# Performance work log

Hardware: AMD Instinct MI355X
Metric: run time of the kernel (lower is better)

The kernel has to match this reference:

```python
import jax, jax.numpy as jnp
import numpy as np

WEIGHT_DIM = 1024
NUM_HEADS = 16
B, L, H = 2, 2048, 1024


def setup_inputs() -> dict:
    key = jax.random.key(0)
    k1, k2, k3, k4, k5 = jax.random.split(key, 5)
    scale = 1.0 / np.sqrt(H)
    return {
        "input": jax.random.normal(k1, (B, L, H), dtype=jnp.float32),
        "attention_mask": jnp.ones((B, L), dtype=jnp.float32),
        "wq": jax.random.normal(k2, (H, WEIGHT_DIM), dtype=jnp.float32) * scale,
        "wk": jax.random.normal(k3, (H, WEIGHT_DIM), dtype=jnp.float32) * scale,
        "wv": jax.random.normal(k4, (H, WEIGHT_DIM), dtype=jnp.float32) * scale,
        "wo": jax.random.normal(k5, (WEIGHT_DIM, H), dtype=jnp.float32) * scale,
    }


def _split_heads(x):
    # (B, L, D) -> (B, nh, L, D/nh)
    b, l, d = x.shape
    return x.reshape(b, l, NUM_HEADS, d // NUM_HEADS).transpose(0, 2, 1, 3)


def reference(input, attention_mask, wq, wk, wv, wo):
    b, l, h = input.shape
    q = _split_heads(input @ wq)
    k = _split_heads(input @ wk)
    v = _split_heads(input @ wv)

    # logits: (B, nh, L, L)
    logit = jnp.einsum("bhqd,bhkd->bhqk", q, k)

    # future mask: strictly upper triangular = 1 (masked)
    f_mask = jnp.triu(jnp.ones((l, l), dtype=jnp.float32), k=1)
    # pad mask: 1 where either position is pad
    p = attention_mask[:, :, None] * attention_mask[:, None, :]  # (B, L, L)
    p_mask = 1.0 - p
    # combined mask (logical_or of booleans expressed as float max)
    mask = jnp.maximum(f_mask[None, None, :, :], p_mask[:, None, :, :])

    # faithful to source: add dtype.min * mask BEFORE dividing by sqrt(d)
    logit = logit + jnp.finfo(logit.dtype).min * mask
    attn = jax.nn.softmax(logit / jnp.sqrt(jnp.float32(WEIGHT_DIM)), axis=-1)

    ctx = jnp.einsum("bhqk,bhkd->bhqd", attn, v)
    ctx = ctx.transpose(0, 2, 1, 3).reshape(b, l, WEIGHT_DIM)
    return ctx @ wo
```

## Files before the change

### kernel.cpp

```cpp
#include <hip/hip_runtime.h>


#define L_SEQ  2048
#define NBATCH 2
#define HDIM   1024
#define NHEADS 16
#define DHEAD  64
#define MB     (L_SEQ)
#define PADK   72
#define PADP   72

using frag_ab = __attribute__((ext_vector_type(8))) short;
using frag_cd = __attribute__((ext_vector_type(4))) float;

__device__ inline unsigned short f2bf(float f) {
  unsigned u = __float_as_uint(f);
  u += 0x7fffu + ((u >> 16) & 1u);
  return (unsigned short)(u >> 16);
}
__device__ inline float bf2f(unsigned short h) {
  return __uint_as_float(((unsigned)h) << 16);
}
__device__ inline float fexp2(float x) {
#if __has_builtin(__builtin_amdgcn_exp2f)
  return __builtin_amdgcn_exp2f(x);
#else
  return exp2f(x);
#endif
}

typedef __attribute__((address_space(1))) unsigned int glb_u32;
typedef __attribute__((address_space(3))) unsigned int lds_u32;
__device__ inline void gload16(const void* g, void* l) {
  __builtin_amdgcn_global_load_lds((glb_u32*)g, (lds_u32*)l, 16, 0, 0);
}

__global__ __launch_bounds__(256) void convx(
    const float* __restrict__ X, unsigned short* __restrict__ Y) {
  size_t idx = ((size_t)blockIdx.x * 256 + threadIdx.x) * 8;
  float4 a = *(const float4*)(X + idx);
  float4 b = *(const float4*)(X + idx + 4);
  union { uint4 v; unsigned short u[8]; } o;
  o.u[0] = f2bf(a.x); o.u[1] = f2bf(a.y); o.u[2] = f2bf(a.z); o.u[3] = f2bf(a.w);
  o.u[4] = f2bf(b.x); o.u[5] = f2bf(b.y); o.u[6] = f2bf(b.z); o.u[7] = f2bf(b.w);
  *(uint4*)(Y + idx) = o.v;
}

__global__ __launch_bounds__(256) void transw(
    const float* wq, const float* wk, const float* wv, const float* wo,
    unsigned short* WT) {
  __shared__ unsigned short t[32][33];
  const float* s = (blockIdx.z == 0) ? wq : (blockIdx.z == 1) ? wk
                 : (blockIdx.z == 2) ? wv : wo;
  unsigned short* d = WT + (size_t)blockIdx.z * HDIM * HDIM;
  int k0 = blockIdx.y * 32, n0 = blockIdx.x * 32;
  int tx = threadIdx.x, ty = threadIdx.y;
  for (int i = ty; i < 32; i += 8)
    t[i][tx] = f2bf(s[(size_t)(k0 + i) * HDIM + n0 + tx]);
  __syncthreads();
  for (int i = ty; i < 32; i += 8)
    d[(size_t)(n0 + i) * HDIM + k0 + tx] = t[tx][i];
}

template<int C_BF16, int VT_OUT>
__global__ __launch_bounds__(256) void gemm128(
    const unsigned short* __restrict__ A,
    const unsigned short* __restrict__ B0, const unsigned short* __restrict__ B1,
    const unsigned short* __restrict__ B2,
    void* __restrict__ C0, void* __restrict__ C1, void* __restrict__ C2) {
  const int K = HDIM, N = HDIM;
  __shared__ __align__(16) unsigned short Sh[2][128 * 64];
  unsigned short* As = &Sh[0][0];
  unsigned short* Bs = &Sh[1][0];
  int tid = threadIdx.x, wave = tid >> 6, lane = tid & 63;
  int quad = lane >> 4, l16 = lane & 15;
  int gid = blockIdx.x;
  int xcd = gid & 7, rest = gid >> 3;
  int mb  = xcd * 4 + (rest & 3);
  int nb  = rest >> 2;
  int m0 = mb * 128;
  const unsigned short* Bt = (nb < 8) ? B0 : (nb < 16) ? B1 : B2;
  void* C = (nb < 8) ? C0 : (nb < 16) ? C1 : C2;
  int n0 = (nb & 7) * 128;
  int wm = wave >> 1, wn = wave & 1;

  frag_cd acc[4][4] = {};

  int lr8 = lane >> 3;
  int cg  = (lane & 7) ^ lr8;
  for (int k0 = 0; k0 < K; k0 += 64) {
    __syncthreads();
#pragma unroll
    for (int i = 0; i < 4; i++) {
      int r8 = wave * 32 + i * 8;
      gload16(A  + (size_t)(m0 + r8 + lr8) * K + k0 + cg * 8, &As[r8 * 64]);
      gload16(Bt + (size_t)(n0 + r8 + lr8) * K + k0 + cg * 8, &Bs[r8 * 64]);
    }
    __syncthreads();
#pragma unroll
    for (int kc = 0; kc < 2; kc++) {
      int ch = ((kc * 4 + quad) ^ (l16 & 7)) * 8;
      frag_ab af[4], bf[4];
#pragma unroll
      for (int t = 0; t < 4; t++) {
        af[t] = *(const frag_ab*)&As[(wm * 64 + t * 16 + l16) * 64 + ch];
        bf[t] = *(const frag_ab*)&Bs[(wn * 64 + t * 16 + l16) * 64 + ch];
      }
#pragma unroll
      for (int mt = 0; mt < 4; mt++)
#pragma unroll
        for (int nt = 0; nt < 4; nt++)
          acc[mt][nt] = __builtin_amdgcn_mfma_f32_16x16x32_bf16(
              af[mt], bf[nt], acc[mt][nt], 0, 0, 0);
    }
  }
  if (VT_OUT && nb >= 16) {
    __syncthreads();
    unsigned short* Tr = &Sh[0][0];
#pragma unroll
    for (int mt = 0; mt < 4; mt++)
#pragma unroll
      for (int nt = 0; nt < 4; nt++) {
        int d  = wn * 64 + nt * 16 + l16;
        int c4 = ((wm * 64 + mt * 16 + quad * 4) >> 2) ^ ((d & 7) << 2);
        ushort4 o;
        o.x = f2bf(acc[mt][nt][0]); o.y = f2bf(acc[mt][nt][1]);
        o.z = f2bf(acc[mt][nt][2]); o.w = f2bf(acc[mt][nt][3]);
        *(ushort4*)&Tr[d * 128 + c4 * 4] = o;
      }
    __syncthreads();
    unsigned short* VTp = (unsigned short*)C;
    int bb = m0 >> 11, key0 = m0 & 2047;
#pragma unroll
    for (int it = 0; it < 8; it++) {
      int d  = wave * 32 + it * 4 + quad;
      int c4 = (l16 * 2) ^ ((d & 7) << 2);
      uint4 v = *(const uint4*)&Tr[d * 128 + c4 * 4];
      int dg = n0 + d;
      size_t addr = ((size_t)((bb * NHEADS + (dg >> 6)) * DHEAD + (dg & 63))) * L_SEQ
                  + key0 + l16 * 8;
      *(uint4*)(VTp + addr) = v;
    }
  } else {
#pragma unroll
    for (int mt = 0; mt < 4; mt++)
#pragma unroll
      for (int nt = 0; nt < 4; nt++)
#pragma unroll
        for (int r = 0; r < 4; r++) {
          int row = m0 + wm * 64 + mt * 16 + quad * 4 + r;
          int col = n0 + wn * 64 + nt * 16 + l16;
          if (C_BF16)
            ((unsigned short*)C)[(size_t)row * N + col] = f2bf(acc[mt][nt][r]);
          else
            ((float*)C)[(size_t)row * N + col] = acc[mt][nt][r];
        }
  }
}

__global__ __launch_bounds__(256) void gemm_proj(
    const unsigned short* __restrict__ A,
    const unsigned short* __restrict__ Bt,
    float* __restrict__ C) {
  const int K = HDIM, N = HDIM;
  __shared__ __align__(16) unsigned short As[128 * 64];
  __shared__ __align__(16) unsigned short Bs[64 * 64];
  int tid = threadIdx.x, wave = tid >> 6, lane = tid & 63;
  int quad = lane >> 4, l16 = lane & 15;
  int gid = blockIdx.x;
  int xcd = gid & 7, rest = gid >> 3;
  int mb  = xcd * 4 + (rest & 3);
  int nbk = rest >> 2;
  int m0 = mb * 128, n0 = nbk * 64;
  int wm = wave >> 1, wn = wave & 1;
  frag_cd acc[4][2] = {};
  int lr8 = lane >> 3, cg = (lane & 7) ^ lr8;
  for (int k0 = 0; k0 < K; k0 += 64) {
    __syncthreads();
#pragma unroll
    for (int i = 0; i < 4; i++) {
      int r8 = wave * 32 + i * 8;
      gload16(A + (size_t)(m0 + r8 + lr8) * K + k0 + cg * 8, &As[r8 * 64]);
    }
#pragma unroll
    for (int j = 0; j < 2; j++) {
      int r8 = wave * 16 + j * 8;
      gload16(Bt + (size_t)(n0 + r8 + lr8) * K + k0 + cg * 8, &Bs[r8 * 64]);
    }
    __syncthreads();
#pragma unroll
    for (int kc = 0; kc < 2; kc++) {
      int ch = ((kc * 4 + quad) ^ (l16 & 7)) * 8;
      frag_ab af[4], bf[2];
#pragma unroll
      for (int t = 0; t < 4; t++)
        af[t] = *(const frag_ab*)&As[(wm * 64 + t * 16 + l16) * 64 + ch];
#pragma unroll
      for (int t = 0; t < 2; t++)
        bf[t] = *(const frag_ab*)&Bs[(wn * 32 + t * 16 + l16) * 64 + ch];
#pragma unroll
      for (int mt = 0; mt < 4; mt++)
#pragma unroll
        for (int nt = 0; nt < 2; nt++)
          acc[mt][nt] = __builtin_amdgcn_mfma_f32_16x16x32_bf16(
              af[mt], bf[nt], acc[mt][nt], 0, 0, 0);
    }
  }
#pragma unroll
  for (int mt = 0; mt < 4; mt++)
#pragma unroll
    for (int nt = 0; nt < 2; nt++)
#pragma unroll
      for (int r = 0; r < 4; r++) {
        int row = m0 + wm * 64 + mt * 16 + quad * 4 + r;
        int col = n0 + wn * 32 + nt * 16 + l16;
        C[(size_t)row * N + col] = acc[mt][nt][r];
      }
}

__global__ __launch_bounds__(256) void attn_st(
    const unsigned short* Qm, const unsigned short* Km,
    const unsigned short* VT, unsigned short* CTX) {
  __shared__ __align__(16) unsigned short Ks[2][64 * 64];
  __shared__ __align__(16) unsigned short Vt[2][64 * 64];
  __shared__ __align__(16) unsigned short Ps[4][16 * PADP];

  int tid = threadIdx.x, wave = tid >> 6, lane = tid & 63;
  int quad = lane >> 4, l16 = lane & 15;
  int gid = blockIdx.x;
  int xcd = gid & 7, g = gid >> 3;
  int combo = xcd + 8 * (g & 3);
  int p = g >> 2;
  int h = combo & 15, b = combo >> 4;
  size_t base  = (size_t)b * L_SEQ * HDIM + (size_t)h * DHEAD;
  size_t vbase = ((size_t)(b * NHEADS + h)) * DHEAD * L_SEQ;
  int lr8 = lane >> 3, cg = (lane & 7) ^ lr8;
  unsigned short* ps = &Ps[wave][0];

  for (int pass = 0; pass < 2; pass++) {
    int qb = (pass == 0) ? p : 31 - p;
    int q0 = qb * 64;
    int ntiles = qb + 1;

    __syncthreads();

    frag_ab qf0, qf1;
    {
      const unsigned short* qp =
          Qm + base + (size_t)(q0 + wave * 16 + l16) * HDIM + quad * 8;
      qf0 = *(const frag_ab*)qp;
      qf1 = *(const frag_ab*)(qp + 32);
      const float QSC = 0.03125f * 1.44269504f;
#pragma unroll
      for (int i = 0; i < 8; i++) {
        qf0[i] = (short)f2bf(bf2f((unsigned short)qf0[i]) * QSC);
        qf1[i] = (short)f2bf(bf2f((unsigned short)qf1[i]) * QSC);
      }
    }

#pragma unroll
    for (int jj = 0; jj < 2; jj++) {
      int r8 = wave * 16 + jj * 8;
      gload16(Km + base + (size_t)(r8 + lr8) * HDIM + cg * 8, &Ks[0][r8 * 64]);
      gload16(VT + vbase + (size_t)(r8 + lr8) * L_SEQ + cg * 8, &Vt[0][r8 * 64]);
    }

    float l_part = 0.f;
    frag_cd acc[4] = {};

    for (int kt = 0; kt < ntiles; kt++) {
      int cur = kt & 1, nxt = cur ^ 1;
      __syncthreads();

      if (kt + 1 < ntiles) {
#pragma unroll
        for (int jj = 0; jj < 2; jj++) {
          int r8 = wave * 16 + jj * 8;
          gload16(Km + base + (size_t)((kt + 1) * 64 + r8 + lr8) * HDIM + cg * 8,
                  &Ks[nxt][r8 * 64]);
          gload16(VT + vbase + (size_t)(r8 + lr8) * L_SEQ + (kt + 1) * 64 + cg * 8,
                  &Vt[nxt][r8 * 64]);
        }
      }

      frag_cd st[4];
#pragma unroll
      for (int kt4 = 0; kt4 < 4; kt4++) {
        frag_ab kf0 = *(const frag_ab*)
            &Ks[cur][(kt4 * 16 + l16) * 64 + ((quad ^ (l16 & 7)) * 8)];
        frag_ab kf1 = *(const frag_ab*)
            &Ks[cur][(kt4 * 16 + l16) * 64 + (((4 + quad) ^ (l16 & 7)) * 8)];
        frag_cd z = {};
        z = __builtin_amdgcn_mfma_f32_16x16x32_bf16(kf0, qf0, z, 0, 0, 0);
        st[kt4] = __builtin_amdgcn_mfma_f32_16x16x32_bf16(kf1, qf1, z, 0, 0, 0);
      }

      if (kt == ntiles - 1) {
        int qrel = wave * 16 + l16;
#pragma unroll
        for (int kt4 = 0; kt4 < 4; kt4++) {
          int keyrel = kt4 * 16 + quad * 4;
#pragma unroll
          for (int r = 0; r < 4; r++)
            if (keyrel + r > qrel) st[kt4][r] = -1e30f;
        }
      }

#pragma unroll
      for (int kt4 = 0; kt4 < 4; kt4++) {
        float p0 = fexp2(st[kt4][0]), p1 = fexp2(st[kt4][1]);
        float p2 = fexp2(st[kt4][2]), p3 = fexp2(st[kt4][3]);
        ushort4 o;
        o.x = f2bf(p0); o.y = f2bf(p1); o.z = f2bf(p2); o.w = f2bf(p3);
        *(ushort4*)&ps[l16 * PADP + kt4 * 16 + quad * 4] = o;
        l_part += (p0 + p1) + (p2 + p3);
      }

#pragma unroll
      for (int c = 0; c < 2; c++) {
        frag_ab pf = *(const frag_ab*)&ps[l16 * PADP + c * 32 + quad * 8];
#pragma unroll
        for (int dt = 0; dt < 4; dt++) {
          frag_ab vf = *(const frag_ab*)
              &Vt[cur][(dt * 16 + l16) * 64 + (((c * 4 + quad) ^ (l16 & 7)) * 8)];
          acc[dt] = __builtin_amdgcn_mfma_f32_16x16x32_bf16(pf, vf, acc[dt], 0, 0, 0);
        }
      }
    }

    l_part += __shfl_xor(l_part, 16);
    l_part += __shfl_xor(l_part, 32);
    float inv = 1.0f / l_part;
    float l_r[4];
#pragma unroll
    for (int r = 0; r < 4; r++)
      l_r[r] = __shfl(inv, quad * 4 + r);

#pragma unroll
    for (int dt = 0; dt < 4; dt++)
#pragma unroll
      for (int r = 0; r < 4; r++) {
        int row = q0 + wave * 16 + quad * 4 + r;
        CTX[base + (size_t)row * HDIM + dt * 16 + l16] = f2bf(acc[dt][r] * l_r[r]);
      }
  }
}

template<int A_BF16, int C_BF16>
__global__ __launch_bounds__(256) void gemm_nn(
    const void* __restrict__ Av, const float* __restrict__ W,
    void* __restrict__ Cv, int M, int N, int K) {
  __shared__ __align__(16) unsigned short As[64][32];
  __shared__ __align__(16) unsigned short Bs[64][32];
  int tid = threadIdx.x;
  int wave = tid >> 6, lane = tid & 63;
  int quad = lane >> 4, l16 = lane & 15;
  int m0 = blockIdx.x * 64, n0 = blockIdx.y * 64;
  frag_cd acc[4] = {};
  int ar = tid >> 2, ac = (tid & 3) * 8;
  int bk = tid >> 3, bn = (tid & 7) * 8;
  for (int k0 = 0; k0 < K; k0 += 32) {
    __syncthreads();
    if (A_BF16) {
      const unsigned short* A = (const unsigned short*)Av;
      *(uint4*)(&As[ar][ac]) = *(const uint4*)(A + (size_t)(m0 + ar) * K + k0 + ac);
    } else {
      const float* A = (const float*)Av;
      const float* ap = A + (size_t)(m0 + ar) * K + k0 + ac;
      float4 f0 = *(const float4*)ap;
      float4 f1 = *(const float4*)(ap + 4);
      unsigned short* d = &As[ar][ac];
      d[0] = f2bf(f0.x); d[1] = f2bf(f0.y); d[2] = f2bf(f0.z); d[3] = f2bf(f0.w);
      d[4] = f2bf(f1.x); d[5] = f2bf(f1.y); d[6] = f2bf(f1.z); d[7] = f2bf(f1.w);
    }
    {
      const float* wp = W + (size_t)(k0 + bk) * N + n0 + bn;
      float4 w0 = *(const float4*)wp;
      float4 w1 = *(const float4*)(wp + 4);
      Bs[bn + 0][bk] = f2bf(w0.x); Bs[bn + 1][bk] = f2bf(w0.y);
      Bs[bn + 2][bk] = f2bf(w0.z); Bs[bn + 3][bk] = f2bf(w0.w);
      Bs[bn + 4][bk] = f2bf(w1.x); Bs[bn + 5][bk] = f2bf(w1.y);
      Bs[bn + 6][bk] = f2bf(w1.z); Bs[bn + 7][bk] = f2bf(w1.w);
    }
    __syncthreads();
    frag_ab a = *(const frag_ab*)(&As[wave * 16 + l16][quad * 8]);
#pragma unroll
    for (int nt = 0; nt < 4; nt++) {
      frag_ab bfr = *(const frag_ab*)(&Bs[nt * 16 + l16][quad * 8]);
      acc[nt] = __builtin_amdgcn_mfma_f32_16x16x32_bf16(a, bfr, acc[nt], 0, 0, 0);
    }
  }
#pragma unroll
  for (int nt = 0; nt < 4; nt++) {
    int col = n0 + nt * 16 + l16;
#pragma unroll
    for (int rr = 0; rr < 4; rr++) {
      int row = m0 + wave * 16 + quad * 4 + rr;
      if (C_BF16)
        ((unsigned short*)Cv)[(size_t)row * N + col] = f2bf(acc[nt][rr]);
      else
        ((float*)Cv)[(size_t)row * N + col] = acc[nt][rr];
    }
  }
}

__global__ __launch_bounds__(256) void attn_mfma(
    const unsigned short* Qm, const unsigned short* Km,
    const unsigned short* Vm, unsigned short* CTX) {
  __shared__ __align__(16) unsigned short Ks[64 * PADK];
  __shared__ __align__(16) unsigned short Vt[64 * PADK];
  __shared__ __align__(16) unsigned short Ps[4][16 * PADK];
  int tid = threadIdx.x;
  int wave = tid >> 6, lane = tid & 63;
  int quad = lane >> 4, l16 = lane & 15;
  int q0 = blockIdx.x * 64;
  int h = blockIdx.y;
  size_t base = (size_t)h * DHEAD;
  int srow = tid >> 2, scol = (tid & 3) * 16;
  {
    const unsigned short* qp = Qm + base + (size_t)(q0 + srow) * HDIM + scol;
    *(uint4*)&Ks[srow * PADK + scol]     = *(const uint4*)qp;
    *(uint4*)&Ks[srow * PADK + scol + 8] = *(const uint4*)(qp + 8);
  }
  __syncthreads();
  frag_ab qf0 = *(const frag_ab*)&Ks[(wave * 16 + l16) * PADK + quad * 8];
  frag_ab qf1 = *(const frag_ab*)&Ks[(wave * 16 + l16) * PADK + 32 + quad * 8];
#pragma unroll
  for (int i = 0; i < 8; i++) {
    qf0[i] = (short)f2bf(bf2f((unsigned short)qf0[i]) * 0.03125f);
    qf1[i] = (short)f2bf(bf2f((unsigned short)qf1[i]) * 0.03125f);
  }
  float m_r[4], l_r[4];
#pragma unroll
  for (int r = 0; r < 4; r++) { m_r[r] = -1e30f; l_r[r] = 0.f; }
  frag_cd acc[4] = {};
  int ntiles = (q0 >> 6) + 1;
  for (int kt = 0; kt < ntiles; kt++) {
    __syncthreads();
    {
      const unsigned short* kp = Km + base + (size_t)(kt * 64 + srow) * HDIM + scol;
      *(uint4*)&Ks[srow * PADK + scol]     = *(const uint4*)kp;
      *(uint4*)&Ks[srow * PADK + scol + 8] = *(const uint4*)(kp + 8);
      const unsigned short* vp = Vm + base + (size_t)(kt * 64 + srow) * HDIM + scol;
      union { uint4 v; unsigned short u[8]; } v0, v1;
      v0.v = *(const uint4*)vp; v1.v = *(const uint4*)(vp + 8);
#pragma unroll
      for (int i = 0; i < 8; i++) {
        Vt[(scol + i) * PADK + srow]     = v0.u[i];
        Vt[(scol + 8 + i) * PADK + srow] = v1.u[i];
      }
    }
    __syncthreads();
    frag_cd s[4];
#pragma unroll
    for (int nt = 0; nt < 4; nt++) {
      frag_ab kf0 = *(const frag_ab*)&Ks[(nt * 16 + l16) * PADK + quad * 8];
      frag_ab kf1 = *(const frag_ab*)&Ks[(nt * 16 + l16) * PADK + 32 + quad * 8];
      frag_cd z = {};
      z = __builtin_amdgcn_mfma_f32_16x16x32_bf16(qf0, kf0, z, 0, 0, 0);
      s[nt] = __builtin_amdgcn_mfma_f32_16x16x32_bf16(qf1, kf1, z, 0, 0, 0);
    }
    if (kt == ntiles - 1) {
      int rowg = wave * 16 + quad * 4;
#pragma unroll
      for (int nt = 0; nt < 4; nt++) {
        int key = nt * 16 + l16;
#pragma unroll
        for (int r = 0; r < 4; r++)
          if (key > rowg + r) s[nt][r] = -1e30f;
      }
    }
    float mnew[4], alpha[4];
#pragma unroll
    for (int r = 0; r < 4; r++) {
      float t = fmaxf(fmaxf(s[0][r], s[1][r]), fmaxf(s[2][r], s[3][r]));
#pragma unroll
      for (int off = 8; off > 0; off >>= 1)
        t = fmaxf(t, __shfl_xor(t, off));
      mnew[r] = fmaxf(m_r[r], t);
      alpha[r] = __expf(m_r[r] - mnew[r]);
      m_r[r] = mnew[r];
    }
    unsigned short* ps = &Ps[wave][0];
#pragma unroll
    for (int nt = 0; nt < 4; nt++)
#pragma unroll
      for (int r = 0; r < 4; r++) {
        float p = __expf(s[nt][r] - mnew[r]);
        s[nt][r] = p;
        ps[(quad * 4 + r) * PADK + nt * 16 + l16] = f2bf(p);
      }
#pragma unroll
    for (int r = 0; r < 4; r++) {
      float t = (s[0][r] + s[1][r]) + (s[2][r] + s[3][r]);
#pragma unroll
      for (int off = 8; off > 0; off >>= 1)
        t += __shfl_xor(t, off);
      l_r[r] = l_r[r] * alpha[r] + t;
    }
#pragma unroll
    for (int nt2 = 0; nt2 < 4; nt2++)
#pragma unroll
      for (int r = 0; r < 4; r++) acc[nt2][r] *= alpha[r];
#pragma unroll
    for (int c = 0; c < 2; c++) {
      frag_ab pf = *(const frag_ab*)&ps[l16 * PADK + c * 32 + quad * 8];
#pragma unroll
      for (int nt2 = 0; nt2 < 4; nt2++) {
        frag_ab vf = *(const frag_ab*)&Vt[(nt2 * 16 + l16) * PADK + c * 32 + quad * 8];
        acc[nt2] = __builtin_amdgcn_mfma_f32_16x16x32_bf16(pf, vf, acc[nt2], 0, 0, 0);
      }
    }
  }
#pragma unroll
  for (int nt2 = 0; nt2 < 4; nt2++)
#pragma unroll
    for (int r = 0; r < 4; r++) {
      int row = q0 + wave * 16 + quad * 4 + r;
      CTX[base + (size_t)row * HDIM + nt2 * 16 + l16] = f2bf(acc[nt2][r] / l_r[r]);
    }
}

extern "C" void kernel_launch(void* const* d_in, const int* in_sizes, int n_in,
                              void* d_out, int out_size, void* d_ws, size_t ws_size,
                              hipStream_t stream) {
  const float* X  = (const float*)d_in[0];
  const float* wq = (const float*)d_in[2];
  const float* wk = (const float*)d_in[3];
  const float* wv = (const float*)d_in[4];
  const float* wo = (const float*)d_in[5];

  const size_t MTOT = (size_t)NBATCH * L_SEQ;
  if (ws_size >= (size_t)24 * 1024 * 1024) {
    unsigned short* Qb = (unsigned short*)d_ws;
    unsigned short* Kb = Qb + MTOT * HDIM;
    unsigned short* WT = Kb + MTOT * HDIM;
    unsigned short* Xb = (unsigned short*)d_out;
    unsigned short* VTb = Xb + MTOT * HDIM;
    float* out = (float*)d_out;
    const size_t WSZ = (size_t)HDIM * HDIM;

    convx<<<2048, 256, 0, stream>>>(X, Xb);
    transw<<<dim3(32, 32, 4), dim3(32, 8), 0, stream>>>(wq, wk, wv, wo, WT);
    gemm128<1, 1><<<768, 256, 0, stream>>>(
        Xb, WT, WT + WSZ, WT + 2 * WSZ, Qb, Kb, VTb);
    attn_st<<<512, 256, 0, stream>>>(Qb, Kb, VTb, Qb);
    gemm_proj<<<512, 256, 0, stream>>>(Qb, WT + 3 * WSZ, out);
  } else {
    float* out = (float*)d_out;
    unsigned short* Qb = (unsigned short*)d_ws;
    unsigned short* Kb = Qb + (size_t)MB * HDIM;
    dim3 ggrid(MB / 64, HDIM / 64);
    dim3 agrid(MB / 64, NHEADS);
    for (int b = 0; b < NBATCH; b++) {
      const float* Xb = X + (size_t)b * MB * HDIM;
      float* outb = out + (size_t)b * MB * HDIM;
      unsigned short* Vb = (unsigned short*)outb;
      gemm_nn<0, 1><<<ggrid, 256, 0, stream>>>(Xb, wq, Qb, MB, HDIM, HDIM);
      gemm_nn<0, 1><<<ggrid, 256, 0, stream>>>(Xb, wk, Kb, MB, HDIM, HDIM);
      gemm_nn<0, 1><<<ggrid, 256, 0, stream>>>(Xb, wv, Vb, MB, HDIM, HDIM);
      attn_mfma<<<agrid, 256, 0, stream>>>(Qb, Kb, Vb, Qb);
      gemm_nn<1, 0><<<ggrid, 256, 0, stream>>>(Qb, wo, outb, MB, HDIM, HDIM);
    }
  }
}
```

Before: 183.7 us.

## Merge prep kernels and compute Q/K/V per block sharing A tile

The X-to-bf16 conversion and the weight transpose are merged into one prep launch, removing one kernel launch. The QKV GEMM now gives each block a 128x64 output tile for all three weights at once. The A tile is loaded once per k-step and reused across Q, K and V, which cuts A reloads from 24 per row block to 16. This raises accumulator register pressure (96 floats) and shrinks the grid from 768 to 512 blocks, so occupancy and the tail behaviour may change.

```diff
diff --git a/kernel.cpp b/kernel.cpp
--- a/kernel.cpp
+++ b/kernel.cpp
@@ -35,126 +35,134 @@
   __builtin_amdgcn_global_load_lds((glb_u32*)g, (lds_u32*)l, 16, 0, 0);
 }
 
-__global__ __launch_bounds__(256) void convx(
-    const float* __restrict__ X, unsigned short* __restrict__ Y) {
-  size_t idx = ((size_t)blockIdx.x * 256 + threadIdx.x) * 8;
-  float4 a = *(const float4*)(X + idx);
-  float4 b = *(const float4*)(X + idx + 4);
-  union { uint4 v; unsigned short u[8]; } o;
-  o.u[0] = f2bf(a.x); o.u[1] = f2bf(a.y); o.u[2] = f2bf(a.z); o.u[3] = f2bf(a.w);
-  o.u[4] = f2bf(b.x); o.u[5] = f2bf(b.y); o.u[6] = f2bf(b.z); o.u[7] = f2bf(b.w);
-  *(uint4*)(Y + idx) = o.v;
-}
-
-__global__ __launch_bounds__(256) void transw(
+__global__ __launch_bounds__(256) void prep(
     const float* wq, const float* wk, const float* wv, const float* wo,
-    unsigned short* WT) {
-  __shared__ unsigned short t[32][33];
-  const float* s = (blockIdx.z == 0) ? wq : (blockIdx.z == 1) ? wk
-                 : (blockIdx.z == 2) ? wv : wo;
-  unsigned short* d = WT + (size_t)blockIdx.z * HDIM * HDIM;
-  int k0 = blockIdx.y * 32, n0 = blockIdx.x * 32;
+    unsigned short* WT, const float* __restrict__ X,
+    unsigned short* __restrict__ Xb) {
+  int z = blockIdx.z;
   int tx = threadIdx.x, ty = threadIdx.y;
-  for (int i = ty; i < 32; i += 8)
-    t[i][tx] = f2bf(s[(size_t)(k0 + i) * HDIM + n0 + tx]);
-  __syncthreads();
-  for (int i = ty; i < 32; i += 8)
-    d[(size_t)(n0 + i) * HDIM + k0 + tx] = t[tx][i];
-}
-
-template<int C_BF16, int VT_OUT>
-__global__ __launch_bounds__(256) void gemm128(
+  if (z < 4) {
+    __shared__ unsigned short t[32][33];
+    const float* s = (z == 0) ? wq : (z == 1) ? wk : (z == 2) ? wv : wo;
+    unsigned short* d = WT + (size_t)z * HDIM * HDIM;
+    int k0 = blockIdx.y * 32, n0 = blockIdx.x * 32;
+    for (int i = ty; i < 32; i += 8)
+      t[i][tx] = f2bf(s[(size_t)(k0 + i) * HDIM + n0 + tx]);
+    __syncthreads();
+    for (int i = ty; i < 32; i += 8)
+      d[(size_t)(n0 + i) * HDIM + k0 + tx] = t[tx][i];
+  } else {
+    size_t blk = (size_t)(z - 4) * 1024 + blockIdx.y * 32 + blockIdx.x;
+    size_t idx = (blk * 256 + ty * 32 + tx) * 8;
+    float4 a = *(const float4*)(X + idx);
+    float4 b = *(const float4*)(X + idx + 4);
+    union { uint4 v; unsigned short u[8]; } o;
+    o.u[0] = f2bf(a.x); o.u[1] = f2bf(a.y); o.u[2] = f2bf(a.z); o.u[3] = f2bf(a.w);
+    o.u[4] = f2bf(b.x); o.u[5] = f2bf(b.y); o.u[6] = f2bf(b.z); o.u[7] = f2bf(b.w);
+    *(uint4*)(Xb + idx) = o.v;
+  }
+}
+
+__global__ __launch_bounds__(256) void gemm_qkv(
     const unsigned short* __restrict__ A,
-    const unsigned short* __restrict__ B0, const unsigned short* __restrict__ B1,
-    const unsigned short* __restrict__ B2,
-    void* __restrict__ C0, void* __restrict__ C1, void* __restrict__ C2) {
-  const int K = HDIM, N = HDIM;
-  __shared__ __align__(16) unsigned short Sh[2][128 * 64];
-  unsigned short* As = &Sh[0][0];
-  unsigned short* Bs = &Sh[1][0];
+    const unsigned short* __restrict__ Bq, const unsigned short* __restrict__ Bk,
+    const unsigned short* __restrict__ Bv,
+    unsigned short* __restrict__ Q, unsigned short* __restrict__ K,
+    unsigned short* __restrict__ VT) {
+  const int KD = HDIM, N = HDIM;
+  __shared__ __align__(16) unsigned short As[128 * 64];
+  __shared__ __align__(16) unsigned short Bs[3][64 * 64];
   int tid = threadIdx.x, wave = tid >> 6, lane = tid & 63;
   int quad = lane >> 4, l16 = lane & 15;
   int gid = blockIdx.x;
   int xcd = gid & 7, rest = gid >> 3;
   int mb  = xcd * 4 + (rest & 3);
-  int nb  = rest >> 2;
-  int m0 = mb * 128;
-  const unsigned short* Bt = (nb < 8) ? B0 : (nb < 16) ? B1 : B2;
-  void* C = (nb < 8) ? C0 : (nb < 16) ? C1 : C2;
-  int n0 = (nb & 7) * 128;
+  int nbk = rest >> 2;
+  int m0 = mb * 128, n0 = nbk * 64;
   int wm = wave >> 1, wn = wave & 1;
 
-  frag_cd acc[4][4] = {};
+  frag_cd acc[3][4][2] = {};
 
   int lr8 = lane >> 3;
   int cg  = (lane & 7) ^ lr8;
-  for (int k0 = 0; k0 < K; k0 += 64) {
+  for (int k0 = 0; k0 < KD; k0 += 64) {
     __syncthreads();
 #pragma unroll
     for (int i = 0; i < 4; i++) {
       int r8 = wave * 32 + i * 8;
-      gload16(A  + (size_t)(m0 + r8 + lr8) * K + k0 + cg * 8, &As[r8 * 64]);
-      gload16(Bt + (size_t)(n0 + r8 + lr8) * K + k0 + cg * 8, &Bs[r8 * 64]);
+      gload16(A + (size_t)(m0 + r8 + lr8) * KD + k0 + cg * 8, &As[r8 * 64]);
+    }
+#pragma unroll
+    for (int j = 0; j < 2; j++) {
+      int r8 = wave * 16 + j * 8;
+      size_t off = (size_t)(n0 + r8 + lr8) * KD + k0 + cg * 8;
+      gload16(Bq + off, &Bs[0][r8 * 64]);
+      gload16(Bk + off, &Bs[1][r8 * 64]);
+      gload16(Bv + off, &Bs[2][r8 * 64]);
     }
     __syncthreads();
 #pragma unroll
     for (int kc = 0; kc < 2; kc++) {
       int ch = ((kc * 4 + quad) ^ (l16 & 7)) * 8;
-      frag_ab af[4], bf[4];
-#pragma unroll
-      for (int t = 0; t < 4; t++) {
+      frag_ab af[4];
+#pragma unroll
+      for (int t = 0; t < 4; t++)
         af[t] = *(const frag_ab*)&As[(wm * 64 + t * 16 + l16) * 64 + ch];
-        bf[t] = *(const frag_ab*)&Bs[(wn * 64 + t * 16 + l16) * 64 + ch];
-      }
-#pragma unroll
-      for (int mt = 0; mt < 4; mt++)
-#pragma unroll
-        for (int nt = 0; nt < 4; nt++)
-          acc[mt][nt] = __builtin_amdgcn_mfma_f32_16x16x32_bf16(
-              af[mt], bf[nt], acc[mt][nt], 0, 0, 0);
-    }
-  }
-  if (VT_OUT && nb >= 16) {
-    __syncthreads();
-    unsigned short* Tr = &Sh[0][0];
-#pragma unroll
-    for (int mt = 0; mt < 4; mt++)
-#pragma unroll
-      for (int nt = 0; nt < 4; nt++) {
-        int d  = wn * 64 + nt * 16 + l16;
-        int c4 = ((wm * 64 + mt * 16 + quad * 4) >> 2) ^ ((d & 7) << 2);
-        ushort4 o;
-        o.x = f2bf(acc[mt][nt][0]); o.y = f2bf(acc[mt][nt][1]);
-        o.z = f2bf(acc[mt][nt][2]); o.w = f2bf(acc[mt][nt][3]);
-        *(ushort4*)&Tr[d * 128 + c4 * 4] = o;
-      }
-    __syncthreads();
-    unsigned short* VTp = (unsigned short*)C;
+#pragma unroll
+      for (int w = 0; w < 3; w++) {
+        frag_ab bf[2];
+#pragma unroll
+        for (int t = 0; t < 2; t++)
+          bf[t] = *(const frag_ab*)&Bs[w][(wn * 32 + t * 16 + l16) * 64 + ch];
+#pragma unroll
+        for (int mt = 0; mt < 4; mt++)
+#pragma unroll
+          for (int nt = 0; nt < 2; nt++)
+            acc[w][mt][nt] = __builtin_amdgcn_mfma_f32_16x16x32_bf16(
+                af[mt], bf[nt], acc[w][mt][nt], 0, 0, 0);
+      }
+    }
+  }
+
+#pragma unroll
+  for (int mt = 0; mt < 4; mt++)
+#pragma unroll
+    for (int nt = 0; nt < 2; nt++)
+#pragma unroll
+      for (int r = 0; r < 4; r++) {
+        int row = m0 + wm * 64 + mt * 16 + quad * 4 + r;
+        int col = n0 + wn * 32 + nt * 16 + l16;
+        Q[(size_t)row * N + col] = f2bf(acc[0][mt][nt][r]);
+        K[(size_t)row * N + col] = f2bf(acc[1][mt][nt][r]);
+      }
+
+  __syncthreads();
+  unsigned short* Tr = &As[0];
+#pragma unroll
+  for (int mt = 0; mt < 4; mt++)
+#pragma unroll
+    for (int nt = 0; nt < 2; nt++) {
+      int d  = wn * 32 + nt * 16 + l16;
+      int kl = wm * 64 + mt * 16 + quad * 4;
+      int c4 = (kl >> 2) ^ ((d & 7) << 2);
+      ushort4 o;
+      o.x = f2bf(acc[2][mt][nt][0]); o.y = f2bf(acc[2][mt][nt][1]);
+      o.z = f2bf(acc[2][mt][nt][2]); o.w = f2bf(acc[2][mt][nt][3]);
+      *(ushort4*)&Tr[d * 128 + c4 * 4] = o;
+    }
+  __syncthreads();
+  {
     int bb = m0 >> 11, key0 = m0 & 2047;
 #pragma unroll
-    for (int it = 0; it < 8; it++) {
-      int d  = wave * 32 + it * 4 + quad;
+    for (int it = 0; it < 4; it++) {
+      int d  = wave * 16 + it * 4 + quad;
       int c4 = (l16 * 2) ^ ((d & 7) << 2);
       uint4 v = *(const uint4*)&Tr[d * 128 + c4 * 4];
       int dg = n0 + d;
       size_t addr = ((size_t)((bb * NHEADS + (dg >> 6)) * DHEAD + (dg & 63))) * L_SEQ
                   + key0 + l16 * 8;
-      *(uint4*)(VTp + addr) = v;
-    }
-  } else {
-#pragma unroll
-    for (int mt = 0; mt < 4; mt++)
-#pragma unroll
-      for (int nt = 0; nt < 4; nt++)
-#pragma unroll
-        for (int r = 0; r < 4; r++) {
-          int row = m0 + wm * 64 + mt * 16 + quad * 4 + r;
-          int col = n0 + wn * 64 + nt * 16 + l16;
-          if (C_BF16)
-            ((unsigned short*)C)[(size_t)row * N + col] = f2bf(acc[mt][nt][r]);
-          else
-            ((float*)C)[(size_t)row * N + col] = acc[mt][nt][r];
-        }
+      *(uint4*)(VT + addr) = v;
+    }
   }
 }
 
@@ -540,9 +548,8 @@
     float* out = (float*)d_out;
     const size_t WSZ = (size_t)HDIM * HDIM;
 
-    convx<<<2048, 256, 0, stream>>>(X, Xb);
-    transw<<<dim3(32, 32, 4), dim3(32, 8), 0, stream>>>(wq, wk, wv, wo, WT);
-    gemm128<1, 1><<<768, 256, 0, stream>>>(
+    prep<<<dim3(32, 32, 6), dim3(32, 8), 0, stream>>>(wq, wk, wv, wo, WT, X, Xb);
+    gemm_qkv<<<512, 256, 0, stream>>>(
         Xb, WT, WT + WSZ, WT + 2 * WSZ, Qb, Kb, VTb);
     attn_st<<<512, 256, 0, stream>>>(Qb, Kb, VTb, Qb);
     gemm_proj<<<512, 256, 0, stream>>>(Qb, WT + 3 * WSZ, out);
```

Result: faster. 169.1 us (-8.0%).
